# Kernel optimization log

Measured on AMD Instinct MI355X. Metric: run time of the kernel, lower is better.

## Reference

```python
import jax, jax.numpy as jnp
from jax import lax
import numpy as np

N = 4
ALPHA_AP = 0.85
ALPHA_DS = 0.1
ALPHA_LR = 1.0
C1 = 0.01 ** 2
C2 = 0.03 ** 2


def resize_ac(img, nh, nw):
    # bilinear resize, align_corners=True (matches F.interpolate(..., align_corners=True))
    B, C, H, W = img.shape
    ys = jnp.linspace(0.0, H - 1.0, nh)
    xs = jnp.linspace(0.0, W - 1.0, nw)
    y0 = jnp.floor(ys).astype(jnp.int32)
    y1 = jnp.minimum(y0 + 1, H - 1)
    x0 = jnp.floor(xs).astype(jnp.int32)
    x1 = jnp.minimum(x0 + 1, W - 1)
    wy = (ys - y0).astype(img.dtype)[None, None, :, None]
    wx = (xs - x0).astype(img.dtype)[None, None, None, :]
    top = img[:, :, y0, :] * (1.0 - wy) + img[:, :, y1, :] * wy
    return top[:, :, :, x0] * (1.0 - wx) + top[:, :, :, x1] * wx


def build_pyramid(img):
    B, C, H, W = img.shape
    pyr = [img]
    for i in range(N - 1):
        r = 2 ** (i + 1)
        pyr.append(resize_ac(pyr[i], H // r, W // r))  # resize previous level, as in torch code
    return pyr


def x_grad(img):
    # replicate-pad right then diff -> last column is exactly zero
    g = img[:, :, :, :-1] - img[:, :, :, 1:]
    return jnp.concatenate([g, jnp.zeros_like(img[:, :, :, :1])], axis=3)


def y_grad(img):
    g = img[:, :, :-1, :] - img[:, :, 1:, :]
    return jnp.concatenate([g, jnp.zeros_like(img[:, :, :1, :])], axis=2)


def avgpool3(x):
    # AvgPool2d(3, 1), VALID padding
    return lax.reduce_window(x, 0.0, lax.add, (1, 1, 3, 3), (1, 1, 1, 1), 'VALID') / 9.0


def grid_sample_zeros(img, gx, gy):
    # bilinear grid_sample, padding_mode='zeros', align_corners=True
    B, C, H, W = img.shape
    x = (gx + 1.0) * 0.5 * (W - 1)
    y = (gy + 1.0) * 0.5 * (H - 1)
    x0 = jnp.floor(x)
    y0 = jnp.floor(y)

    def corner(xi, yi, w):
        valid = (xi >= 0) & (xi <= W - 1) & (yi >= 0) & (yi <= H - 1)
        xc = jnp.clip(xi, 0, W - 1).astype(jnp.int32)
        yc = jnp.clip(yi, 0, H - 1).astype(jnp.int32)
        vals = jax.vmap(lambda im, yy, xx: im[:, yy, xx])(img, yc, xc)  # [B,C,H,W]
        return vals * (w * valid.astype(img.dtype))[:, None]

    return (corner(x0, y0, (x0 + 1 - x) * (y0 + 1 - y))
            + corner(x0 + 1, y0, (x - x0) * (y0 + 1 - y))
            + corner(x0, y0 + 1, (x0 + 1 - x) * (y - y0))
            + corner(x0 + 1, y0 + 1, (x - x0) * (y - y0)))


def apply_disparity(img, disp):
    # standard Monodepth bilinear sampler: shift x_base in [0,1] by disp, grid_sample
    B, C, H, W = img.shape
    x_base = jnp.linspace(0.0, 1.0, W)[None, None, :]
    y_base = jnp.linspace(0.0, 1.0, H)[None, :, None]
    gx = 2.0 * (x_base + disp[:, 0]) - 1.0  # [B,H,W]
    gy = jnp.broadcast_to(2.0 * y_base - 1.0, gx.shape)
    return grid_sample_zeros(img, gx, gy)


def dssim(x, y):
    mu_x = avgpool3(x)
    mu_y = avgpool3(y)
    sig_x = avgpool3(x * x) - mu_x ** 2
    sig_y = avgpool3(y * y) - mu_y ** 2
    cov = avgpool3(x * y) - mu_x * mu_y
    ssim = ((2.0 * mu_x * mu_y + C1) * (2.0 * cov + C2)) / ((mu_x ** 2 + mu_y ** 2 + C1) * (sig_x + sig_y + C2))
    return jnp.mean(jnp.clip((1.0 - ssim) / 2.0, 0.0, 1.0))


def smoothness(disp, img, level):
    wx = jnp.exp(-jnp.mean(jnp.abs(x_grad(img)), axis=1, keepdims=True))
    wy = jnp.exp(-jnp.mean(jnp.abs(y_grad(img)), axis=1, keepdims=True))
    sx = x_grad(disp) * wx
    sy = y_grad(disp) * wy
    return jnp.mean(jnp.abs(sx) + jnp.abs(sy)) / (2 ** level)


def loss_forward(disps, left, right):
    lp = build_pyramid(left)
    rp = build_pyramid(right)
    dl = [d[:, 0:1] for d in disps]
    dr = [d[:, 1:2] for d in disps]
    left_est = [apply_disparity(rp[i], -dl[i]) for i in range(N)]
    right_est = [apply_disparity(lp[i], dr[i]) for i in range(N)]
    r2l_disp = [apply_disparity(dr[i], -dl[i]) for i in range(N)]
    l2r_disp = [apply_disparity(dl[i], dr[i]) for i in range(N)]
    # appearance matching (note: outer *ALPHA_AP matches the original's AP_loss*self.alpha_AP)
    AP = sum(ALPHA_AP * dssim(lp[i], left_est[i]) + (1.0 - ALPHA_AP) * jnp.mean(jnp.abs(lp[i] - left_est[i])) for i in range(N))
    AP = AP + sum(ALPHA_AP * dssim(rp[i], right_est[i]) + (1.0 - ALPHA_AP) * jnp.mean(jnp.abs(rp[i] - right_est[i])) for i in range(N))
    AP = AP * ALPHA_AP
    LR = sum(jnp.mean(jnp.abs(dl[i] - r2l_disp[i])) for i in range(N))
    LR = (LR + sum(jnp.mean(jnp.abs(dr[i] - l2r_disp[i])) for i in range(N))) * ALPHA_LR
    DS = sum(smoothness(dl[i], lp[i], i) for i in range(N))
    DS = (DS + sum(smoothness(dr[i], rp[i], i) for i in range(N))) * ALPHA_DS
    total = AP + LR + DS
    return total, AP, LR, DS


def setup_inputs() -> dict:
    key = jax.random.key(0)
    ks = jax.random.split(key, 6)
    B, H, W = 32, 256, 512
    inp = {}
    for i in range(N):
        h, w = H >> i, W >> i
        # normalized disparities in [0, 0.05) as in trained Monodepth
        inp[f'disp{i}'] = jax.random.uniform(ks[i], (B, 2, h, w), jnp.float32) * 0.05
    inp['left'] = jax.random.uniform(ks[4], (B, 3, H, W), jnp.float32)
    inp['right'] = jax.random.uniform(ks[5], (B, 3, H, W), jnp.float32)
    return inp


def reference(disp0, disp1, disp2, disp3, left, right):
    return loss_forward([disp0, disp1, disp2, disp3], left, right)
```

## Files before the change

### kernel.cpp

```cpp
#include <hip/hip_runtime.h>

#define BDIM 256
#define SH 16

typedef float v2f __attribute__((ext_vector_type(2)));

struct LevelDesc {
    const float* lp; const float* rp; const float* dp;
    int H, W, nCW, nRS, nPerSide, waveBase;
};
struct AllParams { LevelDesc lv[4]; int totalWaves; };

__device__ __forceinline__ float dpp_shl1(float x) {
    int r = __builtin_amdgcn_update_dpp(0, __float_as_int(x), 0x130, 0xF, 0xF, true);
    return __int_as_float(r);
}

__device__ __forceinline__ const float* uptr(const float* p) {
    unsigned long long u = (unsigned long long)p;
    unsigned lo = __builtin_amdgcn_readfirstlane((unsigned)u);
    unsigned hi = __builtin_amdgcn_readfirstlane((unsigned)(u >> 32));
    return (const float*)(((unsigned long long)hi << 32) | (unsigned long long)lo);
}

__device__ __forceinline__ v2f mkv(float a, float b) { v2f r; r.x = a; r.y = b; return r; }


__global__ void resize2_kernel(const float* __restrict__ sL, const float* __restrict__ sR,
                               float* __restrict__ dL, float* __restrict__ dR,
                               int BC, int Hs, int Ws, int Hd, int Wd,
                               double* acc, int doZero) {
    if (doZero && blockIdx.x == 0 && threadIdx.x < 32) acc[threadIdx.x] = 0.0;
    long long half = (long long)BC * Hd * Wd;
    long long idx = (long long)blockIdx.x * blockDim.x + threadIdx.x;
    if (idx >= 2 * half) return;
    const float* src = (idx < half) ? sL : sR;
    float* dst = (idx < half) ? dL : dR;
    long long id = (idx < half) ? idx : idx - half;
    int i = (int)(id % Wd);
    long long t = id / Wd;
    int j = (int)(t % Hd);
    int bc = (int)(t / Hd);
    float stepy = (float)(Hs - 1) / (float)(Hd - 1);
    float stepx = (float)(Ws - 1) / (float)(Wd - 1);
    float y = j * stepy;
    float x = i * stepx;
    int y0 = (int)floorf(y);
    int y1 = min(y0 + 1, Hs - 1);
    int x0 = (int)floorf(x);
    int x1 = min(x0 + 1, Ws - 1);
    float wy = y - (float)y0;
    float wx = x - (float)x0;
    const float* s = src + (long long)bc * Hs * Ws;
    float t0 = s[(long long)y0 * Ws + x0] * (1.0f - wy) + s[(long long)y1 * Ws + x0] * wy;
    float t1 = s[(long long)y0 * Ws + x1] * (1.0f - wy) + s[(long long)y1 * Ws + x1] * wy;
    dst[id] = t0 * (1.0f - wx) + t1 * wx;
}

__device__ __forceinline__ v2f ssim_term2(v2f Sx, v2f Sy, v2f Sxx, v2f Syy, v2f Sxy) {
    const float C1v = 0.0001f;
    const float C2v = 0.0009f;
    const float i9 = 1.0f / 9.0f;
    v2f mux = Sx * i9, muy = Sy * i9;
    v2f sigx = Sxx * i9 - mux * mux;
    v2f sigy = Syy * i9 - muy * muy;
    v2f cov  = Sxy * i9 - mux * muy;
    v2f num = ((2.0f * mux) * muy + C1v) * (2.0f * cov + C2v);
    v2f den = (mux * mux + muy * muy + C1v) * (sigx + sigy + C2v);
    v2f r;
    r.x = __builtin_amdgcn_rcpf(den.x);
    r.y = __builtin_amdgcn_rcpf(den.y);
    v2f v = (1.0f - num * r) * 0.5f;
    v2f o;
    o.x = __builtin_amdgcn_fmed3f(v.x, 0.0f, 1.0f);
    o.y = __builtin_amdgcn_fmed3f(v.y, 0.0f, 1.0f);
    return o;
}

struct RowVals {
    float d0, d1;
    v2f xv[3];
    v2f wI, wJ;
    v2f dI, dJ;
    v2f sI[3], sJ[3];
};

__global__ void __launch_bounds__(BDIM)
mega_kernel(AllParams P, double* __restrict__ acc) {
    const int lane = threadIdx.x & 63;
    const int wid  = threadIdx.x >> 6;
    const int wId  = blockIdx.x * (BDIM / 64) + wid;
    const int w = min(wId, P.totalWaves - 1);

    int level = 0;
    if (w >= P.lv[1].waveBase) level = 1;
    if (w >= P.lv[2].waveBase) level = 2;
    if (w >= P.lv[3].waveBase) level = 3;
    LevelDesc L;
    if (level == 0) L = P.lv[0];
    else if (level == 1) L = P.lv[1];
    else if (level == 2) L = P.lv[2];
    else L = P.lv[3];

    int rel = w - L.waveBase;
    const int side = (rel >= L.nPerSide) ? 1 : 0;
    rel -= side * L.nPerSide;
    const int cw = rel % L.nCW; rel /= L.nCW;
    const int rs = rel % L.nRS;
    const int b  = rel / L.nRS;

    const int H = L.H, W = L.W;
    const long long HW = (long long)H * W;
    const unsigned HWu = (unsigned)HW;
    const float Wm1f = (float)(W - 1);
    const float sgn = side ? 1.0f : -1.0f;

    const float* xim = uptr((side ? L.rp : L.lp) + (long long)b * 3 * HW);
    const float* sim = uptr((side ? L.lp : L.rp) + (long long)b * 3 * HW);
    const float* dme = uptr(L.dp + (long long)b * 2 * HW + (side ? HW : 0));
    const float* dot = uptr(L.dp + (long long)b * 2 * HW + (side ? 0 : HW));

    const int base = cw * 126;
    const int c0 = base + 2 * lane;
    const int c1 = c0 + 1;
    const bool in0 = c0 < W, in1 = c1 < W;
    const int cc = min(c0, W - 2) >> 1;
    const float fc0 = (float)c0, fc1 = (float)c1;

    const bool lastW = (cw == L.nCW - 1);
    const bool own0 = in0 && (c0 < base + 126 || lastW);
    const bool own1 = in1 && (c1 < base + 126 || lastW);
    const bool ownS0 = own0 && (c0 <= W - 3);
    const bool ownS1 = own1 && (c1 <= W - 3);

    const float mO0 = own0 ? 1.f : 0.f, mO1 = own1 ? 1.f : 0.f;
    const float mS0 = ownS0 ? 1.f : 0.f, mS1 = ownS1 ? 1.f : 0.f;
    const float mX0 = (own0 && c0 < W - 1) ? 1.f : 0.f;
    const float mX1 = (own1 && c1 < W - 1) ? 1.f : 0.f;

    const int r0 = rs * SH;
    const int r1 = min(r0 + SH, H);
    const int jend = min(r1 + 1, H - 1);

    v2f Pst[3][5], Lst[3][5];
#pragma unroll
    for (int c = 0; c < 3; ++c)
#pragma unroll
        for (int s = 0; s < 5; ++s) { Pst[c][s] = mkv(0.f, 0.f); Lst[c][s] = mkv(0.f, 0.f); }
    float pd0 = 0.f, pd1 = 0.f;
    v2f pxv[3] = {mkv(0.f,0.f), mkv(0.f,0.f), mkv(0.f,0.f)};

    float f_ss = 0.f, f_l1 = 0.f, f_lr = 0.f, f_ds = 0.f;

    auto load_dp = [&](int jj, float& o0, float& o1) {
        float2 dpair = ((const float2*)(dme + (unsigned)jj * (unsigned)W))[cc];
        o0 = dpair.x; o1 = dpair.y;
    };

    auto issue_gathers = [&](float di0, float di1, int jj, RowVals& R) {
        const unsigned ro = (unsigned)jj * (unsigned)W;
        R.d0 = di0; R.d1 = di1;
        float xq0 = fmaf(sgn * di0, Wm1f, fc0);
        float xq1 = fmaf(sgn * di1, Wm1f, fc1);
        float xf0 = floorf(xq0), xf1 = floorf(xq1);
        int g0 = (int)xf0, g1 = (int)xf1;
        float t0 = xq0 - xf0, t1 = xq1 - xf1;
        float w00 = (in0 && g0 >= 0 && g0 < W)         ? 1.0f - t0 : 0.0f;
        float w01 = (in0 && g0 >= -1 && g0 < W - 1)    ? t0        : 0.0f;
        float w10 = (in1 && g1 >= 0 && g1 < W)         ? 1.0f - t1 : 0.0f;
        float w11 = (in1 && g1 >= -1 && g1 < W - 1)    ? t1        : 0.0f;
        R.wI = mkv(w00, w10);
        R.wJ = mkv(w01, w11);
        unsigned a0 = ro + (unsigned)min(max(g0, 0), W - 1);
        unsigned a1 = ro + (unsigned)min(max(g0 + 1, 0), W - 1);
        unsigned b0 = ro + (unsigned)min(max(g1, 0), W - 1);
        unsigned b1 = ro + (unsigned)min(max(g1 + 1, 0), W - 1);
        R.dI = mkv(dot[a0], dot[b0]);
        R.dJ = mkv(dot[a1], dot[b1]);
#pragma unroll
        for (int c = 0; c < 3; ++c) {
            const unsigned co = (unsigned)c * HWu;
            float2 xp2 = ((const float2*)(xim + co + ro))[cc];
            R.xv[c] = mkv(in0 ? xp2.x : 0.f, in1 ? xp2.y : 0.f);
            R.sI[c] = mkv(sim[co + a0], sim[co + b0]);
            R.sJ[c] = mkv(sim[co + a1], sim[co + b1]);
        }
    };

    auto consume = [&](const RowVals& R, int j) {
        const float d0 = R.d0, d1 = R.d1;
        v2f wv2 = R.dI * R.wI + R.dJ * R.wJ;
        v2f xv[3], yv[3];
#pragma unroll
        for (int c = 0; c < 3; ++c) {
            xv[c] = R.xv[c];
            yv[c] = R.sI[c] * R.wI + R.sJ[c] * R.wJ;
        }

        const bool rowOwn = j < r1;
        if (rowOwn) {
            float s0 = fabsf(xv[0].x - yv[0].x) + fabsf(xv[1].x - yv[1].x) + fabsf(xv[2].x - yv[2].x);
            float s1 = fabsf(xv[0].y - yv[0].y) + fabsf(xv[1].y - yv[1].y) + fabsf(xv[2].y - yv[2].y);
            f_l1 = fmaf(mO0, s0, f_l1);
            f_l1 = fmaf(mO1, s1, f_l1);
            f_lr = fmaf(mO0, fabsf(d0 - wv2.x), f_lr);
            f_lr = fmaf(mO1, fabsf(d1 - wv2.y), f_lr);
        }

        {
            float dn  = dpp_shl1(d0);
            float xn0 = dpp_shl1(xv[0].x);
            float xn1 = dpp_shl1(xv[1].x);
            float xn2 = dpp_shl1(xv[2].x);
            if (rowOwn) {
                float g0v = fabsf(xv[0].x - xv[0].y) + fabsf(xv[1].x - xv[1].y) + fabsf(xv[2].x - xv[2].y);
                float g1v = fabsf(xv[0].y - xn0) + fabsf(xv[1].y - xn1) + fabsf(xv[2].y - xn2);
                f_ds = fmaf(mX0, fabsf((d0 - d1) * __expf(-g0v * (1.0f / 3.0f))), f_ds);
                f_ds = fmaf(mX1, fabsf((d1 - dn) * __expf(-g1v * (1.0f / 3.0f))), f_ds);
            }
        }
        if (j > r0 && (j - 1) < r1) {
            v2f t0 = pxv[0] - xv[0];
            v2f t1 = pxv[1] - xv[1];
            v2f t2 = pxv[2] - xv[2];
            float g0v = fabsf(t0.x) + fabsf(t1.x) + fabsf(t2.x);
            float g1v = fabsf(t0.y) + fabsf(t1.y) + fabsf(t2.y);
            f_ds = fmaf(mO0, fabsf((pd0 - d0) * __expf(-g0v * (1.0f / 3.0f))), f_ds);
            f_ds = fmaf(mO1, fabsf((pd1 - d1) * __expf(-g1v * (1.0f / 3.0f))), f_ds);
        }
        pd0 = d0; pd1 = d1;
#pragma unroll
        for (int c = 0; c < 3; ++c) pxv[c] = xv[c];

        const bool emit = (j >= r0 + 2);
#pragma unroll
        for (int c = 0; c < 3; ++c) {
            v2f X = xv[c], Y = yv[c];
            v2f V[5];
            V[0] = X; V[1] = Y;
            V[2] = X * X; V[3] = Y * Y; V[4] = X * Y;
            v2f cs[5];
#pragma unroll
            for (int s = 0; s < 5; ++s) {
                cs[s] = Pst[c][s] + V[s];
                Pst[c][s] = Lst[c][s] + V[s];
                Lst[c][s] = V[s];
            }
            if (emit) {
                v2f Wn[5];
#pragma unroll
                for (int s = 0; s < 5; ++s) {
                    float s0 = cs[s].x + cs[s].y;
                    Wn[s].x = s0 + dpp_shl1(cs[s].x);
                    Wn[s].y = cs[s].y + dpp_shl1(s0);
                }
                v2f ts = ssim_term2(Wn[0], Wn[1], Wn[2], Wn[3], Wn[4]);
                f_ss = fmaf(mS0, ts.x, f_ss);
                f_ss = fmaf(mS1, ts.y, f_ss);
            }
        }
    };

    RowVals A, B;
    float dq0, dq1, dn0, dn1;
    load_dp(r0, dq0, dq1);
    load_dp(min(r0 + 1, jend), dn0, dn1);
    issue_gathers(dq0, dq1, r0, A);

    int j = r0;
    for (;;) {
        float dp20, dp21;
        load_dp(min(j + 2, jend), dp20, dp21);
        if (j < jend) issue_gathers(dn0, dn1, j + 1, B);
        consume(A, j);
        dn0 = dp20; dn1 = dp21;
        if (++j > jend) break;

        load_dp(min(j + 2, jend), dp20, dp21);
        if (j < jend) issue_gathers(dn0, dn1, j + 1, A);
        consume(B, j);
        dn0 = dp20; dn1 = dp21;
        if (++j > jend) break;
    }

#pragma unroll
    for (int o = 32; o > 0; o >>= 1) {
        f_ss += __shfl_down(f_ss, o);
        f_l1 += __shfl_down(f_l1, o);
        f_lr += __shfl_down(f_lr, o);
        f_ds += __shfl_down(f_ds, o);
    }
    __shared__ float red[BDIM / 64][4];
    __shared__ int meta[2];
    if (threadIdx.x == 0) { meta[0] = level; meta[1] = side; }
    if (lane == 0) {
        red[wid][0] = f_ss; red[wid][1] = f_l1;
        red[wid][2] = f_lr; red[wid][3] = f_ds;
    }
    __syncthreads();
    if (threadIdx.x < 4) {
        int t = threadIdx.x;
        double s = (double)red[0][t] + (double)red[1][t]
                 + (double)red[2][t] + (double)red[3][t];
        atomicAdd(acc + t * 8 + meta[1] * 4 + meta[0], s);
    }
}

__global__ void finalize_kernel(const double* __restrict__ acc, float* __restrict__ out) {
    const int B = 32, H0 = 256, W0 = 512;
    double AP = 0.0, LR = 0.0, DS = 0.0;
    for (int i = 0; i < 4; ++i) {
        int h = H0 >> i, w = W0 >> i;
        double nss = (double)B * 3.0 * (double)(h - 2) * (double)(w - 2);
        double nl1 = (double)B * 3.0 * (double)h * (double)w;
        double nd  = (double)B * (double)h * (double)w;
        AP += 0.85 * (acc[0 + i] / nss) + 0.15 * (acc[8 + i] / nl1);
        AP += 0.85 * (acc[4 + i] / nss) + 0.15 * (acc[12 + i] / nl1);
        LR += acc[16 + i] / nd + acc[20 + i] / nd;
        double sc = 1.0 / (double)(1 << i);
        DS += (acc[24 + i] / nd) * sc + (acc[28 + i] / nd) * sc;
    }
    AP *= 0.85;
    DS *= 0.1;
    double total = AP + LR + DS;
    out[0] = (float)total;
    out[1] = (float)AP;
    out[2] = (float)LR;
    out[3] = (float)DS;
}

extern "C" void kernel_launch(void* const* d_in, const int* in_sizes, int n_in,
                              void* d_out, int out_size, void* d_ws, size_t ws_size,
                              hipStream_t stream) {
    const int B = 32, H0 = 256, W0 = 512;
    const float* dsp[4];
    for (int i = 0; i < 4; ++i) dsp[i] = (const float*)d_in[i];
    const float* left  = (const float*)d_in[4];
    const float* right = (const float*)d_in[5];
    float* out = (float*)d_out;

    double* acc = (double*)d_ws;
    float* buf = (float*)((char*)d_ws + 256);

    const float* lp[4];
    const float* rp[4];
    float* lpm[4];
    float* rpm[4];
    lp[0] = left; rp[0] = right;
    float* cur = buf;
    for (int i = 1; i < 4; ++i) { lpm[i] = cur; cur += (long long)B * 3 * (H0 >> i) * (W0 >> i); }
    for (int i = 1; i < 4; ++i) { rpm[i] = cur; cur += (long long)B * 3 * (H0 >> i) * (W0 >> i); }
    for (int i = 1; i < 4; ++i) { lp[i] = lpm[i]; rp[i] = rpm[i]; }

    for (int i = 1; i < 4; ++i) {
        int Hs = H0 >> (i - 1), Ws = W0 >> (i - 1);
        int Hd = H0 >> i, Wd = W0 >> i;
        long long half = (long long)B * 3 * Hd * Wd;
        int g = (int)((2 * half + BDIM - 1) / BDIM);
        resize2_kernel<<<g, BDIM, 0, stream>>>(
            lp[i - 1], rp[i - 1], lpm[i], rpm[i], B * 3, Hs, Ws, Hd, Wd,
            acc, (i == 1) ? 1 : 0);
    }

    AllParams P;
    int wb = 0;
    for (int i = 0; i < 4; ++i) {
        int h = H0 >> i, w = W0 >> i;
        LevelDesc& L = P.lv[i];
        L.lp = lp[i]; L.rp = rp[i]; L.dp = dsp[i];
        L.H = h; L.W = w;
        L.nCW = (w - 2 + 125) / 126;
        L.nRS = h / SH;
        L.nPerSide = B * L.nRS * L.nCW;
        L.waveBase = wb;
        wb += 2 * L.nPerSide;
    }
    P.totalWaves = wb;
    int blocks = (wb + (BDIM / 64) - 1) / (BDIM / 64);
    mega_kernel<<<blocks, BDIM, 0, stream>>>(P, acc);

    finalize_kernel<<<1, 1, 0, stream>>>(acc, out);
}
```

Baseline: 282.4 us.

## Fuse three pyramid resize launches into one kernel recomputing from full-res

Replaces the three sequential resize launches with a single pyramid kernel in which each level-2 and level-3 pixel is recomputed from the full-resolution image through nested bilinear interpolation, with sizes hard-coded as constants. This removes two kernel launches and the serial dependency between levels. In exchange, level 2 costs 16 and level 3 costs 64 full-resolution gathers per output pixel, and the kernel only handles the fixed 32x3x256x512 shape.

```diff
diff --git a/kernel.cpp b/kernel.cpp
--- a/kernel.cpp
+++ b/kernel.cpp
@@ -25,37 +25,79 @@
 
 __device__ __forceinline__ v2f mkv(float a, float b) { v2f r; r.x = a; r.y = b; return r; }
 
-
-__global__ void resize2_kernel(const float* __restrict__ sL, const float* __restrict__ sR,
-                               float* __restrict__ dL, float* __restrict__ dR,
-                               int BC, int Hs, int Ws, int Hd, int Wd,
-                               double* acc, int doZero) {
-    if (doZero && blockIdx.x == 0 && threadIdx.x < 32) acc[threadIdx.x] = 0.0;
-    long long half = (long long)BC * Hd * Wd;
-    long long idx = (long long)blockIdx.x * blockDim.x + threadIdx.x;
-    if (idx >= 2 * half) return;
-    const float* src = (idx < half) ? sL : sR;
-    float* dst = (idx < half) ? dL : dR;
-    long long id = (idx < half) ? idx : idx - half;
-    int i = (int)(id % Wd);
-    long long t = id / Wd;
-    int j = (int)(t % Hd);
-    int bc = (int)(t / Hd);
-    float stepy = (float)(Hs - 1) / (float)(Hd - 1);
-    float stepx = (float)(Ws - 1) / (float)(Wd - 1);
-    float y = j * stepy;
-    float x = i * stepx;
-    int y0 = (int)floorf(y);
-    int y1 = min(y0 + 1, Hs - 1);
-    int x0 = (int)floorf(x);
-    int x1 = min(x0 + 1, Ws - 1);
-    float wy = y - (float)y0;
-    float wx = x - (float)x0;
-    const float* s = src + (long long)bc * Hs * Ws;
-    float t0 = s[(long long)y0 * Ws + x0] * (1.0f - wy) + s[(long long)y1 * Ws + x0] * wy;
-    float t1 = s[(long long)y0 * Ws + x1] * (1.0f - wy) + s[(long long)y1 * Ws + x1] * wy;
-    dst[id] = t0 * (1.0f - wx) + t1 * wx;
-}
+#define S1Y (255.0f / 127.0f)
+#define S1X (511.0f / 255.0f)
+#define S2Y (127.0f / 63.0f)
+#define S2X (255.0f / 127.0f)
+#define S3Y (63.0f / 31.0f)
+#define S3X (127.0f / 63.0f)
+
+__device__ __forceinline__ float bil0(const float* __restrict__ s, int j, int i) {
+    float y = j * S1Y, x = i * S1X;
+    int y0 = (int)floorf(y); int y1 = min(y0 + 1, 255);
+    int x0 = (int)floorf(x); int x1 = min(x0 + 1, 511);
+    float wy = y - (float)y0, wx = x - (float)x0;
+    float t0 = s[y0 * 512 + x0] * (1.0f - wy) + s[y1 * 512 + x0] * wy;
+    float t1 = s[y0 * 512 + x1] * (1.0f - wy) + s[y1 * 512 + x1] * wy;
+    return t0 * (1.0f - wx) + t1 * wx;
+}
+__device__ __forceinline__ float bil1(const float* __restrict__ s, int j, int i) {
+    float y = j * S2Y, x = i * S2X;
+    int y0 = (int)floorf(y); int y1 = min(y0 + 1, 127);
+    int x0 = (int)floorf(x); int x1 = min(x0 + 1, 255);
+    float wy = y - (float)y0, wx = x - (float)x0;
+    float v00 = bil0(s, y0, x0), v10 = bil0(s, y1, x0);
+    float v01 = bil0(s, y0, x1), v11 = bil0(s, y1, x1);
+    float t0 = v00 * (1.0f - wy) + v10 * wy;
+    float t1 = v01 * (1.0f - wy) + v11 * wy;
+    return t0 * (1.0f - wx) + t1 * wx;
+}
+__device__ __forceinline__ float bil2(const float* __restrict__ s, int j, int i) {
+    float y = j * S3Y, x = i * S3X;
+    int y0 = (int)floorf(y); int y1 = min(y0 + 1, 63);
+    int x0 = (int)floorf(x); int x1 = min(x0 + 1, 127);
+    float wy = y - (float)y0, wx = x - (float)x0;
+    float v00 = bil1(s, y0, x0), v10 = bil1(s, y1, x0);
+    float v01 = bil1(s, y0, x1), v11 = bil1(s, y1, x1);
+    float t0 = v00 * (1.0f - wy) + v10 * wy;
+    float t1 = v01 * (1.0f - wy) + v11 * wy;
+    return t0 * (1.0f - wx) + t1 * wx;
+}
+
+__global__ void __launch_bounds__(256)
+pyramid_kernel(const float* __restrict__ left, const float* __restrict__ right,
+               float* __restrict__ l1, float* __restrict__ r1,
+               float* __restrict__ l2, float* __restrict__ r2,
+               float* __restrict__ l3, float* __restrict__ r3,
+               double* acc) {
+    if (blockIdx.x == 0 && threadIdx.x < 32) acc[threadIdx.x] = 0.0;
+    const int n1 = 96 * 128 * 256;
+    const int n2 = 96 * 64 * 128;
+    const int n3 = 96 * 32 * 64;
+    int idx = blockIdx.x * 256 + threadIdx.x;
+    if (idx < 2 * n1) {
+        const float* src = (idx < n1) ? left : right;
+        float* dst = (idx < n1) ? l1 : r1;
+        int id = (idx < n1) ? idx : idx - n1;
+        int i = id & 255, j = (id >> 8) & 127, bc = id >> 15;
+        dst[id] = bil0(src + bc * 131072, j, i);
+    } else if (idx < 2 * n1 + 2 * n2) {
+        int t = idx - 2 * n1;
+        const float* src = (t < n2) ? left : right;
+        float* dst = (t < n2) ? l2 : r2;
+        int id = (t < n2) ? t : t - n2;
+        int i = id & 127, j = (id >> 7) & 63, bc = id >> 13;
+        dst[id] = bil1(src + bc * 131072, j, i);
+    } else if (idx < 2 * n1 + 2 * n2 + 2 * n3) {
+        int t = idx - 2 * n1 - 2 * n2;
+        const float* src = (t < n3) ? left : right;
+        float* dst = (t < n3) ? l3 : r3;
+        int id = (t < n3) ? t : t - n3;
+        int i = id & 63, j = (id >> 6) & 31, bc = id >> 11;
+        dst[id] = bil2(src + bc * 131072, j, i);
+    }
+}
+
 
 __device__ __forceinline__ v2f ssim_term2(v2f Sx, v2f Sy, v2f Sxx, v2f Syy, v2f Sxy) {
     const float C1v = 0.0001f;
@@ -352,14 +394,13 @@
     for (int i = 1; i < 4; ++i) { rpm[i] = cur; cur += (long long)B * 3 * (H0 >> i) * (W0 >> i); }
     for (int i = 1; i < 4; ++i) { lp[i] = lpm[i]; rp[i] = rpm[i]; }
 
-    for (int i = 1; i < 4; ++i) {
-        int Hs = H0 >> (i - 1), Ws = W0 >> (i - 1);
-        int Hd = H0 >> i, Wd = W0 >> i;
-        long long half = (long long)B * 3 * Hd * Wd;
-        int g = (int)((2 * half + BDIM - 1) / BDIM);
-        resize2_kernel<<<g, BDIM, 0, stream>>>(
-            lp[i - 1], rp[i - 1], lpm[i], rpm[i], B * 3, Hs, Ws, Hd, Wd,
-            acc, (i == 1) ? 1 : 0);
+    {
+        int n1 = 96 * 128 * 256, n2 = 96 * 64 * 128, n3 = 96 * 32 * 64;
+        int total = 2 * (n1 + n2 + n3);
+        int g = (total + 255) / 256;
+        pyramid_kernel<<<g, 256, 0, stream>>>(left, right,
+                                              lpm[1], rpm[1], lpm[2], rpm[2],
+                                              lpm[3], rpm[3], acc);
     }
 
     AllParams P;
```

Result: slower. 334.6 us (+18.5%).
